# Kernel optimization log

Measured on AMD Instinct MI355X. Metric: run time of the kernel, lower is better.

The kernel has to match this reference:

```python
import jax, jax.numpy as jnp
import numpy as np

FS = 16000.0
SOUND_SPEED = 343.0
MAX_ORDER = 10
FILTER_LEN = 81            # fractional-delay sinc filter taps (torchaudio default)
PAD = FILTER_LEN // 2      # 40
RIR_LEN = 8000             # static RIR length; bounds max delay for 10 m rooms, order 10

# ---- static image-source lattice: all (i,j,k) with |i|+|j|+|k| <= MAX_ORDER ----
_ind = np.arange(-MAX_ORDER, MAX_ORDER + 1)
_g = np.stack(np.meshgrid(_ind, _ind, _ind, indexing="ij"), -1).reshape(-1, 3)
_g = _g[np.abs(_g).sum(-1) <= MAX_ORDER]                      # (n_img=1561, 3)
XYZ = jnp.asarray(_g, dtype=jnp.float32)                      # (n_img, 3)
EXP_LO = jnp.asarray(np.abs(np.floor(_g / 2.0)), jnp.float32)        # reflections off x=0/y=0/z=0 walls
EXP_HI = jnp.asarray(np.abs(np.floor((_g + 1) / 2.0)), jnp.float32)  # reflections off far walls
ODD = jnp.asarray(_g % 2 == 1)                                # (n_img, 3) bool


def _hann(x, T):
    # truncated Hann window used by the fractional-delay filter
    return jnp.where(jnp.abs(x) <= T / 2, 0.5 * (1.0 + jnp.cos(2.0 * jnp.pi * x / T)), 0.0)


def _rir_one(room, mic, src, absorption):
    # room, mic, src: (3,) metres; absorption: (6,) per-wall absorption coeff
    # image-source positions: mirror source across walls per parity of lattice index
    img = jnp.where(ODD, room * (XYZ + 1.0) - src, room * XYZ + src)   # (n_img, 3)
    tr = jnp.sqrt(1.0 - absorption)                                     # wall reflection coeffs (6,)
    att = jnp.prod((tr[::2] ** EXP_LO) * (tr[1::2] ** EXP_HI), axis=-1)  # (n_img,)
    dist = jnp.linalg.norm(img - mic, axis=-1)                           # (n_img,)
    amp = att / dist                                                     # 1/r spreading
    delay = dist * FS / SOUND_SPEED                                      # delay in samples (float)
    delay_i = jnp.ceil(delay)                                            # integer anchor
    n = jnp.arange(-PAD, PAD + 1, dtype=jnp.float32)                     # (81,)
    x = n[None, :] + delay_i[:, None] - delay[:, None]                   # (n_img, 81)
    irs = amp[:, None] * jnp.sinc(x) * _hann(x, 2 * PAD)                 # windowed-sinc frac delay
    # scatter-add each 81-tap filter at offset delay_i - PAD into the RIR buffer
    idx = delay_i.astype(jnp.int32)[:, None] - PAD + jnp.arange(FILTER_LEN, dtype=jnp.int32)
    valid = (idx >= 0) & (idx < RIR_LEN)
    rir = jnp.zeros((RIR_LEN,), irs.dtype).at[jnp.clip(idx, 0, RIR_LEN - 1)].add(
        jnp.where(valid, irs, 0.0))
    return rir


def setup_inputs() -> dict:
    key = jax.random.key(0)
    k1, k2, k3, k4 = jax.random.split(key, 4)
    B = 256
    room = 3.0 + 7.0 * jax.random.uniform(k1, (B, 3), jnp.float32)       # room dims in [3,10] m
    mic_f = 0.05 + 0.40 * jax.random.uniform(k2, (B, 3), jnp.float32)    # mic frac in [0.05,0.45]
    src_f = 0.55 + 0.40 * jax.random.uniform(k3, (B, 3), jnp.float32)    # src frac in [0.55,0.95]
    absorp = 0.1 + 0.4 * jax.random.uniform(k4, (B, 1), jnp.float32)     # absorption in [0.1,0.5]
    inp = jnp.concatenate([room, mic_f, src_f, absorp], axis=1)          # (B, 10)
    return {"input": inp}


def reference(input):
    room = input[:, 0:3]
    mic = input[:, 3:6] * room
    src = input[:, 6:9] * room
    absorption = jnp.repeat(input[:, 9:10], 6, axis=1)                   # uniform over 6 walls
    rir = jax.vmap(_rir_one)(room, mic, src, absorption)                 # (B, RIR_LEN)
    dist = jnp.linalg.norm(mic - src, axis=1)
    toa = 40.0 + FS * dist / SOUND_SPEED                                 # (B,)
    return rir, toa
```

## Files before the change

### kernel.cpp

```cpp
#include <hip/hip_runtime.h>
#include <math.h>

#define NB 256
#define NIMG 1561
#define RIRLEN 8000
#define PADI 40
#define NTHREADS 1024
#define NWAVES (NTHREADS / 64)
#define NBKT 505
#define NSTARTP 512
#define NPAIR 63
#define CHUNK 64
#define MAXITEMS 256

struct ImgTab { unsigned int v[NIMG]; };

constexpr ImgTab build_tab() {
    ImgTab t{};
    int n = 0;
    for (int x = -10; x <= 10; ++x)
        for (int y = -10; y <= 10; ++y)
            for (int z = -10; z <= 10; ++z) {
                int ax = x < 0 ? -x : x;
                int ay = y < 0 ? -y : y;
                int az = z < 0 ? -z : z;
                int l1 = ax + ay + az;
                if (l1 <= 10) {
                    t.v[n++] = (unsigned)(x + 10) | ((unsigned)(y + 10) << 5) |
                               ((unsigned)(z + 10) << 10) | ((unsigned)l1 << 15);
                }
            }
    return t;
}

constexpr int tab_count() {
    int n = 0;
    for (int x = -10; x <= 10; ++x)
        for (int y = -10; y <= 10; ++y)
            for (int z = -10; z <= 10; ++z) {
                int ax = x < 0 ? -x : x;
                int ay = y < 0 ? -y : y;
                int az = z < 0 ? -z : z;
                if (ax + ay + az <= 10) ++n;
            }
    return n;
}
static_assert(tab_count() == NIMG, "image count mismatch");

__constant__ ImgTab c_tab = build_tab();

__global__ __launch_bounds__(NTHREADS) void
rir_kernel(const float* __restrict__ in, float* __restrict__ out) {
    __shared__ float4 s_rec[NIMG + 1];
    __shared__ float  s_out[RIRLEN];
    __shared__ float  s_trpow[11];
    __shared__ int    s_hist[NSTARTP];
    __shared__ int    s_start[NSTARTP];
    __shared__ int    s_cursor[NBKT];
    __shared__ int    s_T;
    __shared__ int    s_qnext;
    __shared__ int    s_nspike;
    __shared__ int    s_spike_idx[64];
    __shared__ float  s_spike_amp[64];

    int* const s_item = s_hist;

    const int b   = blockIdx.x;
    const int tid = threadIdx.x;
    const float* p = in + b * 10;

    if (tid < NSTARTP) s_hist[tid] = 0;
    for (int i = tid; i < RIRLEN; i += NTHREADS) s_out[i] = 0.0f;
    if (tid == 0) {
        float tr = sqrtf(1.0f - p[9]);
        float pw = 1.0f;
        for (int k = 0; k <= 10; ++k) { s_trpow[k] = pw; pw *= tr; }
        s_nspike = 0;
        s_qnext  = NWAVES;
        s_rec[NIMG] = make_float4(0.0f, 0.0f, 0.0f, -1.0e6f);
    }
    __syncthreads();

    const float rx = p[0], ry = p[1], rz = p[2];
    const float mx = p[3] * rx, my = p[4] * ry, mz = p[5] * rz;
    const float sx = p[6] * rx, sy = p[7] * ry, sz = p[8] * rz;
    const float K = 16000.0f / 343.0f;
    const float INV_PI = 0.31830988618379067154f;

    float4 rec[2];
    int ibkt[2]  = {0, 0};
    bool ivalid[2] = {false, false};

    for (int u = 0; u < 2; ++u) {
        int i = tid + u * NTHREADS;
        if (i < NIMG) {
            unsigned v = c_tab.v[i];
            int gx = (int)(v & 31u) - 10;
            int gy = (int)((v >> 5) & 31u) - 10;
            int gz = (int)((v >> 10) & 31u) - 10;
            int l1 = (int)(v >> 15);

            float ix = (gx & 1) ? rx * (float)(gx + 1) - sx : rx * (float)gx + sx;
            float iy = (gy & 1) ? ry * (float)(gy + 1) - sy : ry * (float)gy + sy;
            float iz = (gz & 1) ? rz * (float)(gz + 1) - sz : rz * (float)gz + sz;

            float dx = ix - mx, dy = iy - my, dz = iz - mz;
            float dist = sqrtf(dx * dx + dy * dy + dz * dz);

            float amp  = s_trpow[l1] * __builtin_amdgcn_rcpf(dist);
            float d    = dist * K;
            float dlc  = ceilf(d);
            float frac = dlc - d;
            int   idlc = (int)dlc;
            int   base = idlc - PADI;

            if (base < RIRLEN) {
                if (frac == 0.0f) {
                    if (idlc < RIRLEN) {
                        int sp = atomicAdd(&s_nspike, 1);
                        if (sp < 64) { s_spike_idx[sp] = idlc; s_spike_amp[sp] = amp; }
                    }
                } else {
                    float spf = (frac < 1.0e-3f) ? frac : (sinpif(frac) * INV_PI);
                    float S   = amp * spf;
                    if (idlc & 1) S = -S;
                    float hS  = 0.5f * S;
                    float cd  = cospif(d * 0.025f);
                    float sd  = sinpif(d * 0.025f);
                    rec[u] = make_float4(hS, hS * cd, hS * sd, d);
                    ibkt[u]   = (base + 80) >> 4;
                    ivalid[u] = true;
                    atomicAdd(&s_hist[ibkt[u]], 1);
                }
            }
        }
    }
    __syncthreads();

    if (tid < 64) {
        int base_i = tid * 8;
        int v[8], pre[8];
        int run = 0;
#pragma unroll
        for (int j = 0; j < 8; ++j) {
            v[j] = s_hist[base_i + j];
            pre[j] = run;
            run += v[j];
        }
        int t = run;
#pragma unroll
        for (int d2 = 1; d2 < 64; d2 <<= 1) {
            int y = __shfl_up(t, d2);
            if (tid >= d2) t += y;
        }
        int excl = t - run;
#pragma unroll
        for (int j = 0; j < 8; ++j) {
            int idx = base_i + j;
            int sv  = excl + pre[j];
            s_start[idx] = sv;
            if (idx < NBKT) s_cursor[idx] = sv;
        }
    }
    __syncthreads();

    for (int u = 0; u < 2; ++u) {
        if (ivalid[u]) {
            int pos = atomicAdd(&s_cursor[ibkt[u]], 1);
            s_rec[pos] = rec[u];
        }
    }

    if (tid < 64) {
        int nch = 0, q = 62 - tid;
        if (tid < NPAIR) {
            int lenA = s_start[8 * q + 9]  - s_start[8 * q];
            int lenB = s_start[8 * q + 13] - s_start[8 * q + 4];
            int ml   = (lenA > lenB) ? lenA : lenB;
            nch = (ml + CHUNK - 1) >> 6;
        }
        int run = nch;
#pragma unroll
        for (int d2 = 1; d2 < 64; d2 <<= 1) {
            int y = __shfl_up(run, d2);
            if (tid >= d2) run += y;
        }
        int excl = run - nch;
        int tot  = __shfl(run, 63);
        if (tid == 0) s_T = (tot < MAXITEMS) ? tot : MAXITEMS;
        for (int c = 0; c < nch; ++c)
            if (excl + c < MAXITEMS) s_item[excl + c] = (q << 5) | c;
    }
    __syncthreads();

    const int wave = tid >> 6;
    const int lane = tid & 63;
    const int h    = lane >> 5;
    const int l5   = lane & 31;
    const float sgn = (l5 & 1) ? -1.0f : 1.0f;
    const float c32 = -0.80901699437494742410f;
    const float s32 =  0.58778525229247312917f;
    float* __restrict__ ob = out + (size_t)b * RIRLEN;
    const int T = s_T;

    int idx = wave;
    while (idx < T) {
        const int item = s_item[idx];
        const int q = item >> 5, c = item & 31;
        const int n0 = (q << 7) + (h << 6) + l5;
        const int n1 = n0 + 32;
        const float fn0 = (float)n0;
        const float cn0 = cospif(fn0 * 0.025f), sn0 = sinpif(fn0 * 0.025f);
        const float cnn1 = cn0 * c32 - sn0 * s32;
        const float snn1 = sn0 * c32 + cn0 * s32;

        const int loA = s_start[8 * q];
        const int hiA = s_start[8 * q + 9];
        const int loB = s_start[8 * q + 4];
        const int hiB = s_start[8 * q + 13];
        const int lenA = hiA - loA, lenB = hiB - loB;
        const int lmn = (lenA < lenB) ? lenA : lenB;
        const int lmx = (lenA > lenB) ? lenA : lenB;
        const int st  = c << 6;
        int e0 = lmn - st; e0 = (e0 < 0) ? 0 : ((e0 > CHUNK) ? CHUNK : e0);
        int e1 = lmx - st; e1 = (e1 > CHUNK) ? CHUNK : e1;
        const int lo = (h ? loB : loA) + st;
        const int hi = h ? hiB : hiA;

        float acc0 = 0.0f, acc1 = 0.0f;
#pragma clang loop unroll_count(8)
        for (int it = 0; it < e0; ++it) {
            float4 r = s_rec[lo + it];
            float x0 = fn0 - r.w;
            float x1 = x0 + 32.0f;
            float pr = __builtin_amdgcn_rcpf(x0 * x1);
            float t0 = fmaf(r.y, cn0, r.x);  t0 = fmaf(r.z, sn0, t0);
            float t1 = fmaf(r.y, cnn1, r.x); t1 = fmaf(r.z, snn1, t1);
            t0 = (fabsf(x0) < 40.0f) ? t0 : 0.0f;
            t1 = (fabsf(x1) < 40.0f) ? t1 : 0.0f;
            acc0 = fmaf(t0 * x1, pr, acc0);
            acc1 = fmaf(t1 * x0, pr, acc1);
        }
#pragma clang loop unroll_count(4)
        for (int it = e0; it < e1; ++it) {
            int k = lo + it;
            float4 r = s_rec[(k < hi) ? k : NIMG];
            float x0 = fn0 - r.w;
            float x1 = x0 + 32.0f;
            float pr = __builtin_amdgcn_rcpf(x0 * x1);
            float t0 = fmaf(r.y, cn0, r.x);  t0 = fmaf(r.z, sn0, t0);
            float t1 = fmaf(r.y, cnn1, r.x); t1 = fmaf(r.z, snn1, t1);
            t0 = (fabsf(x0) < 40.0f) ? t0 : 0.0f;
            t1 = (fabsf(x1) < 40.0f) ? t1 : 0.0f;
            acc0 = fmaf(t0 * x1, pr, acc0);
            acc1 = fmaf(t1 * x0, pr, acc1);
        }
        if (n0 < RIRLEN) atomicAdd(&s_out[n0], acc0 * sgn);
        if (n1 < RIRLEN) atomicAdd(&s_out[n1], acc1 * sgn);

        int nq;
        if (lane == 0) nq = atomicAdd(&s_qnext, 1);
        idx = __shfl(nq, 0);
    }

    __syncthreads();
    int nsp = s_nspike; nsp = (nsp < 64) ? nsp : 64;
    if (tid < nsp) atomicAdd(&s_out[s_spike_idx[tid]], s_spike_amp[tid]);
    __syncthreads();

    float4* __restrict__ o4 = (float4*)ob;
    const float4* s4 = (const float4*)s_out;
#pragma unroll 2
    for (int i = tid; i < RIRLEN / 4; i += NTHREADS) o4[i] = s4[i];

    if (tid == 0) {
        float dx = mx - sx, dy = my - sy, dz = mz - sz;
        out[(size_t)NB * RIRLEN + b] = 40.0f + sqrtf(dx * dx + dy * dy + dz * dz) * K;
    }
}

extern "C" void kernel_launch(void* const* d_in, const int* in_sizes, int n_in,
                              void* d_out, int out_size, void* d_ws, size_t ws_size,
                              hipStream_t stream) {
    const float* in = (const float*)d_in[0];
    float* out = (float*)d_out;
    rir_kernel<<<dim3(NB), dim3(NTHREADS), 0, stream>>>(in, out);
}
```

Baseline: 79.35 us.

## Use 8-sample buckets and four 32-sample sub-tiles per wave to tighten gather windows

Image-source records are now bucketed at 8-sample granularity instead of 16, and each wave splits its 128-sample output group into four 32-lane sub-tiles (two outputs per lane, 16 apart) instead of two 64-sample halves. Each sub-tile reads a narrower contiguous record window, so fewer out-of-range taps are evaluated and masked. The histogram and cursor arrays are aliased into the not-yet-zeroed output buffer to save LDS, which adds an extra barrier and moves the zeroing of the output after the scatter. The per-group chunk count is now set by the largest of four windows, which may raise per-item imbalance, and the unroll factors are lowered.

Result: faster. 77.35 us (-2.5%).

```diff
diff --git a/kernel.cpp b/kernel.cpp
--- a/kernel.cpp
+++ b/kernel.cpp
@@ -7,11 +7,10 @@
 #define PADI 40
 #define NTHREADS 1024
 #define NWAVES (NTHREADS / 64)
-#define NBKT 505
-#define NSTARTP 512
-#define NPAIR 63
+#define NBKT8 1024
+#define NGRP 63
 #define CHUNK 64
-#define MAXITEMS 256
+#define MAXITEMS 192
 
 struct ImgTab { unsigned int v[NIMG]; };
 
@@ -53,24 +52,23 @@
 rir_kernel(const float* __restrict__ in, float* __restrict__ out) {
     __shared__ float4 s_rec[NIMG + 1];
     __shared__ float  s_out[RIRLEN];
+    __shared__ int    s_start[NBKT8];
+    __shared__ int    s_item[MAXITEMS];
     __shared__ float  s_trpow[11];
-    __shared__ int    s_hist[NSTARTP];
-    __shared__ int    s_start[NSTARTP];
-    __shared__ int    s_cursor[NBKT];
     __shared__ int    s_T;
     __shared__ int    s_qnext;
     __shared__ int    s_nspike;
     __shared__ int    s_spike_idx[64];
     __shared__ float  s_spike_amp[64];
 
-    int* const s_item = s_hist;
+    int* const s_hist   = (int*)s_out;
+    int* const s_cursor = (int*)s_out + 1024;
 
     const int b   = blockIdx.x;
     const int tid = threadIdx.x;
     const float* p = in + b * 10;
 
-    if (tid < NSTARTP) s_hist[tid] = 0;
-    for (int i = tid; i < RIRLEN; i += NTHREADS) s_out[i] = 0.0f;
+    if (tid < NBKT8) s_hist[tid] = 0;
     if (tid == 0) {
         float tr = sqrtf(1.0f - p[9]);
         float pw = 1.0f;
@@ -128,7 +126,7 @@
                     float cd  = cospif(d * 0.025f);
                     float sd  = sinpif(d * 0.025f);
                     rec[u] = make_float4(hS, hS * cd, hS * sd, d);
-                    ibkt[u]   = (base + 80) >> 4;
+                    ibkt[u]   = ((base + 40) >> 3) + 5;
                     ivalid[u] = true;
                     atomicAdd(&s_hist[ibkt[u]], 1);
                 }
@@ -138,14 +136,14 @@
     __syncthreads();
 
     if (tid < 64) {
-        int base_i = tid * 8;
-        int v[8], pre[8];
+        int base_i = tid * 16;
+        int pre[16];
         int run = 0;
 #pragma unroll
-        for (int j = 0; j < 8; ++j) {
-            v[j] = s_hist[base_i + j];
+        for (int j = 0; j < 16; ++j) {
+            int v = s_hist[base_i + j];
             pre[j] = run;
-            run += v[j];
+            run += v;
         }
         int t = run;
 #pragma unroll
@@ -155,11 +153,11 @@
         }
         int excl = t - run;
 #pragma unroll
-        for (int j = 0; j < 8; ++j) {
+        for (int j = 0; j < 16; ++j) {
             int idx = base_i + j;
             int sv  = excl + pre[j];
-            s_start[idx] = sv;
-            if (idx < NBKT) s_cursor[idx] = sv;
+            s_start[idx]  = sv;
+            s_cursor[idx] = sv;
         }
     }
     __syncthreads();
@@ -170,13 +168,19 @@
             s_rec[pos] = rec[u];
         }
     }
+    __syncthreads();
 
     if (tid < 64) {
-        int nch = 0, q = 62 - tid;
-        if (tid < NPAIR) {
-            int lenA = s_start[8 * q + 9]  - s_start[8 * q];
-            int lenB = s_start[8 * q + 13] - s_start[8 * q + 4];
-            int ml   = (lenA > lenB) ? lenA : lenB;
+        int nch = 0, g = 62 - tid;
+        if (tid < NGRP) {
+            int bs = 16 * g;
+            int l0 = s_start[bs + 14] - s_start[bs];
+            int l1 = s_start[bs + 18] - s_start[bs + 4];
+            int l2 = s_start[bs + 22] - s_start[bs + 8];
+            int l3 = s_start[bs + 26] - s_start[bs + 12];
+            int ml = (l0 > l1) ? l0 : l1;
+            ml = (l2 > ml) ? l2 : ml;
+            ml = (l3 > ml) ? l3 : ml;
             nch = (ml + CHUNK - 1) >> 6;
         }
         int run = nch;
@@ -189,50 +193,51 @@
         int tot  = __shfl(run, 63);
         if (tid == 0) s_T = (tot < MAXITEMS) ? tot : MAXITEMS;
         for (int c = 0; c < nch; ++c)
-            if (excl + c < MAXITEMS) s_item[excl + c] = (q << 5) | c;
-    }
+            if (excl + c < MAXITEMS) s_item[excl + c] = (g << 5) | c;
+    }
+    for (int i = tid; i < RIRLEN; i += NTHREADS) s_out[i] = 0.0f;
     __syncthreads();
 
     const int wave = tid >> 6;
     const int lane = tid & 63;
-    const int h    = lane >> 5;
-    const int l5   = lane & 31;
-    const float sgn = (l5 & 1) ? -1.0f : 1.0f;
-    const float c32 = -0.80901699437494742410f;
-    const float s32 =  0.58778525229247312917f;
+    const int j    = lane >> 4;
+    const int l4   = lane & 15;
+    const float sgn = (l4 & 1) ? -1.0f : 1.0f;
+    const float c16 = 0.30901699437494742410f;
+    const float s16 = 0.95105651629515357212f;
     float* __restrict__ ob = out + (size_t)b * RIRLEN;
     const int T = s_T;
 
     int idx = wave;
     while (idx < T) {
         const int item = s_item[idx];
-        const int q = item >> 5, c = item & 31;
-        const int n0 = (q << 7) + (h << 6) + l5;
-        const int n1 = n0 + 32;
+        const int g = item >> 5, c = item & 31;
+        const int n0 = (g << 7) + (j << 5) + l4;
+        const int n1 = n0 + 16;
         const float fn0 = (float)n0;
         const float cn0 = cospif(fn0 * 0.025f), sn0 = sinpif(fn0 * 0.025f);
-        const float cnn1 = cn0 * c32 - sn0 * s32;
-        const float snn1 = sn0 * c32 + cn0 * s32;
-
-        const int loA = s_start[8 * q];
-        const int hiA = s_start[8 * q + 9];
-        const int loB = s_start[8 * q + 4];
-        const int hiB = s_start[8 * q + 13];
-        const int lenA = hiA - loA, lenB = hiB - loB;
-        const int lmn = (lenA < lenB) ? lenA : lenB;
-        const int lmx = (lenA > lenB) ? lenA : lenB;
+        const float cnn1 = cn0 * c16 - sn0 * s16;
+        const float snn1 = sn0 * c16 + cn0 * s16;
+
+        const int bs = 16 * g;
+        const int l0 = s_start[bs + 14] - s_start[bs];
+        const int l1 = s_start[bs + 18] - s_start[bs + 4];
+        const int l2 = s_start[bs + 22] - s_start[bs + 8];
+        const int l3 = s_start[bs + 26] - s_start[bs + 12];
+        int lmn = (l0 < l1) ? l0 : l1; lmn = (l2 < lmn) ? l2 : lmn; lmn = (l3 < lmn) ? l3 : lmn;
+        int lmx = (l0 > l1) ? l0 : l1; lmx = (l2 > lmx) ? l2 : lmx; lmx = (l3 > lmx) ? l3 : lmx;
         const int st  = c << 6;
         int e0 = lmn - st; e0 = (e0 < 0) ? 0 : ((e0 > CHUNK) ? CHUNK : e0);
         int e1 = lmx - st; e1 = (e1 > CHUNK) ? CHUNK : e1;
-        const int lo = (h ? loB : loA) + st;
-        const int hi = h ? hiB : hiA;
+        const int lo = s_start[bs + 4 * j] + st;
+        const int hi = s_start[bs + 4 * j + 14];
 
         float acc0 = 0.0f, acc1 = 0.0f;
-#pragma clang loop unroll_count(8)
+#pragma clang loop unroll_count(4)
         for (int it = 0; it < e0; ++it) {
             float4 r = s_rec[lo + it];
             float x0 = fn0 - r.w;
-            float x1 = x0 + 32.0f;
+            float x1 = x0 + 16.0f;
             float pr = __builtin_amdgcn_rcpf(x0 * x1);
             float t0 = fmaf(r.y, cn0, r.x);  t0 = fmaf(r.z, sn0, t0);
             float t1 = fmaf(r.y, cnn1, r.x); t1 = fmaf(r.z, snn1, t1);
@@ -241,12 +246,12 @@
             acc0 = fmaf(t0 * x1, pr, acc0);
             acc1 = fmaf(t1 * x0, pr, acc1);
         }
-#pragma clang loop unroll_count(4)
+#pragma clang loop unroll_count(2)
         for (int it = e0; it < e1; ++it) {
             int k = lo + it;
             float4 r = s_rec[(k < hi) ? k : NIMG];
             float x0 = fn0 - r.w;
-            float x1 = x0 + 32.0f;
+            float x1 = x0 + 16.0f;
             float pr = __builtin_amdgcn_rcpf(x0 * x1);
             float t0 = fmaf(r.y, cn0, r.x);  t0 = fmaf(r.z, sn0, t0);
             float t1 = fmaf(r.y, cnn1, r.x); t1 = fmaf(r.z, snn1, t1);
```
